# Optimization experiments

Hardware: AMD Instinct MI355X
Metric: run time of the kernel (lower is better)

## Reference

```python
import jax, jax.numpy as jnp
import numpy as np

H = 4
N = 50000
D_IN = 128
D_MODEL = 256
NCLASS = 40
B_S = 1
BH = B_S * H
LN_EPS = 1e-5


def sparse_perm_1D(indices, values, feats, n, bh):
    """Batched sparse (bh,n,n) @ dense (bh,n,d): gather -> scale -> segment-sum scatter."""
    gathered = feats[indices[0], indices[2]]              # (nnz, d)
    contrib = values[:, None] * gathered                   # (nnz, d)
    seg = indices[0] * n + indices[1]                      # (nnz,)
    out = jax.ops.segment_sum(contrib, seg, num_segments=bh * n)
    return out.reshape(bh, n, -1)


def layer_norm(x, gamma, beta):
    mu = jnp.mean(x, axis=-1, keepdims=True)
    var = jnp.var(x, axis=-1, keepdims=True)
    return (x - mu) * jax.lax.rsqrt(var + LN_EPS) * gamma + beta


def setup_inputs() -> dict:
    key = jax.random.key(0)
    k1, k2, k3, k4, k5, k6, k7 = jax.random.split(key, 7)
    # per-(batch*head) permutation sigma: nonzero at (b, i, sigma_b(i))
    perm_keys = jax.random.split(k1, BH)
    sigma = jax.vmap(lambda k: jax.random.permutation(k, N))(perm_keys)  # (BH, N)
    b_idx = jnp.repeat(jnp.arange(BH), N)
    row_idx = jnp.tile(jnp.arange(N), BH)
    col_idx = sigma.reshape(-1)
    perm_indices = jnp.stack([b_idx, row_idx, col_idx], axis=0).astype(jnp.int32)  # (3, BH*N)
    perm_values = jax.random.uniform(k2, (BH * N,), dtype=jnp.float32)
    features = jax.random.normal(k3, (B_S, N, D_IN), dtype=jnp.float32)
    appd = jax.random.normal(k4, (B_S, N, D_IN), dtype=jnp.float32)
    # parameters
    w_scale_in = 1.0 / np.sqrt(2 * D_IN)
    W_in = jax.random.uniform(k5, (2 * D_IN, D_MODEL), dtype=jnp.float32, minval=-w_scale_in, maxval=w_scale_in)
    b_in = jnp.zeros((D_MODEL,), dtype=jnp.float32)
    ln_gamma = jnp.ones((D_MODEL * H,), dtype=jnp.float32)
    ln_beta = jnp.zeros((D_MODEL * H,), dtype=jnp.float32)
    w_scale_h = 1.0 / np.sqrt(D_MODEL * H)
    W_head = jax.random.uniform(k6, (D_MODEL * H, NCLASS), dtype=jnp.float32, minval=-w_scale_h, maxval=w_scale_h)
    b_head = jax.random.uniform(k7, (NCLASS,), dtype=jnp.float32, minval=-w_scale_h, maxval=w_scale_h)
    return {"perm_indices": perm_indices, "perm_values": perm_values,
            "features": features, "appd": appd,
            "W_in": W_in, "b_in": b_in,
            "ln_gamma": ln_gamma, "ln_beta": ln_beta,
            "W_head": W_head, "b_head": b_head}


def reference(perm_indices, perm_values, features, appd, W_in, b_in, ln_gamma, ln_beta, W_head, b_head):
    # concat auxiliary features, replicate per head: (B_S,N,2*D_IN) -> (BH,N,2*D_IN)
    feat = jnp.concatenate([features, appd], axis=-1)
    feat = jnp.broadcast_to(feat[:, None], (B_S, H, N, 2 * D_IN)).reshape(BH, N, 2 * D_IN)
    # permute rows: perm @ feat
    x = sparse_perm_1D(perm_indices, perm_values, feat, N, BH)
    # ff_in + relu (dropout is identity at eval)
    x = jax.nn.relu(x @ W_in + b_in)                       # (BH, N, D_MODEL)
    # nlayers == nblocks == 0: compress/uncompress loops are empty
    # inverse permutation: perm^T @ x (swap row/col indices)
    idx_t = jnp.stack([perm_indices[0], perm_indices[2], perm_indices[1]], axis=0)
    y = sparse_perm_1D(idx_t, perm_values, x, N, BH)       # (BH, N, D_MODEL)
    # (B_S,H,N,D) -> (B_S,N,H*D)
    y = y.reshape(B_S, H, N, D_MODEL).transpose(0, 2, 1, 3).reshape(B_S, N, H * D_MODEL)
    y = layer_norm(y, ln_gamma, ln_beta)
    return y @ W_head + b_head                             # (B_S, N, NCLASS)
```

## Files before the change

kernel.cpp:

```cpp
#include <hip/hip_runtime.h>
#include <hip/hip_bf16.h>

#define NROW 50000
#define DIN 128
#define DM 256
#define HH 4
#define NC 40
#define BHN 200000
#define NBLK 3125

typedef float f32x4 __attribute__((ext_vector_type(4)));
typedef short bf16x8 __attribute__((ext_vector_type(8)));

__device__ __forceinline__ unsigned short f2bf(float x) {
    unsigned int u = __float_as_uint(x);
    u += 0x7fffu + ((u >> 16) & 1u);
    return (unsigned short)(u >> 16);
}

__device__ __forceinline__ unsigned int pk2(float lo, float hi) {
    __hip_bfloat162 h = __float22bfloat162_rn(make_float2(lo, hi));
    return *(unsigned int*)&h;
}

__device__ __forceinline__ float bf2f(unsigned short s) {
    return __uint_as_float(((unsigned int)s) << 16);
}

__global__ __launch_bounds__(256) void k_prep(const int* __restrict__ pi,
                                              const float* __restrict__ pv,
                                              const float* __restrict__ Win,
                                              const float* __restrict__ Wh,
                                              const float* __restrict__ gamma,
                                              const float* __restrict__ beta,
                                              const float* __restrict__ bh,
                                              float* __restrict__ vcol,
                                              unsigned short* __restrict__ Wpk,
                                              unsigned short* __restrict__ Wgpk,
                                              float* __restrict__ bias2) {
    const int bid = blockIdx.x, tid = threadIdx.x;
    if (bid < 782) {
        int k = bid * 256 + tid;
        if (k < BHN) {
            int b = (k >= 150000) ? 3 : (k >= 100000) ? 2 : (k >= 50000) ? 1 : 0;
            int col = pi[2 * BHN + k];
            vcol[b * NROW + col] = pv[k];
        }
    } else if (bid < 798) {
        int base = (bid - 782) * 512;
        #pragma unroll
        for (int q = 0; q < 2; ++q) {
            int s = base + q * 256 + tid;
            int ln = s & 63;
            int t  = (s >> 6) & 15;
            int kc = s >> 10;
            int n  = t * 16 + (ln & 15);
            int kb = kc * 32 + ((ln >> 4) << 3);
            union { unsigned int ui[4]; uint4 v4; } u;
            #pragma unroll
            for (int jj = 0; jj < 4; ++jj)
                u.ui[jj] = pk2(Win[(kb + 2 * jj) * DM + n], Win[(kb + 2 * jj + 1) * DM + n]);
            *(uint4*)&Wpk[s * 8] = u.v4;
        }
    } else if (bid < 810) {
        int base = (bid - 798) * 512;
        #pragma unroll
        for (int q = 0; q < 2; ++q) {
            int s = base + q * 256 + tid;
            int ln = s & 63;
            int u6 = s >> 6;
            int t  = u6 % 3;
            int v6 = u6 / 3;
            int kc = v6 & 7;
            int h  = v6 >> 3;
            int c  = t * 16 + (ln & 15);
            int d0 = h * 256 + kc * 32 + ((ln >> 4) << 3);
            union { unsigned int ui[4]; uint4 v4; } u;
            if (c < NC) {
                #pragma unroll
                for (int jj = 0; jj < 4; ++jj)
                    u.ui[jj] = pk2(gamma[d0 + 2 * jj] * Wh[(d0 + 2 * jj) * NC + c],
                                   gamma[d0 + 2 * jj + 1] * Wh[(d0 + 2 * jj + 1) * NC + c]);
            } else {
                u.v4 = make_uint4(0u, 0u, 0u, 0u);
            }
            *(uint4*)&Wgpk[s * 8] = u.v4;
        }
    } else {
        __shared__ float red[256];
        int c = bid - 810;
        float sb = 0.f;
        #pragma unroll
        for (int q = 0; q < 4; ++q) {
            int d = tid + 256 * q;
            sb = fmaf(beta[d], Wh[d * NC + c], sb);
        }
        red[tid] = sb;
        __syncthreads();
        for (int st = 128; st > 0; st >>= 1) {
            if (tid < st) red[tid] += red[tid + st];
            __syncthreads();
        }
        if (tid == 0) bias2[c] = bh[c] + red[0];
    }
}

__global__ __launch_bounds__(64, 3) void k_fused(
    const float* __restrict__ feats, const float* __restrict__ appd,
    const unsigned short* __restrict__ Wpk,
    const unsigned short* __restrict__ Wgpk,
    const float* __restrict__ vcol,
    const float* __restrict__ b_in,
    const float* __restrict__ bias2,
    float* __restrict__ out)
{
    __shared__ __align__(16) unsigned short Gb[16 * 264];
    __shared__ float rsS[16], nmS[16];

    const int tid = threadIdx.x;
    const int quad = tid >> 4;
    const int lr = tid & 15;
    const int j0 = blockIdx.x * 16;
    const int ar = j0 + lr;

    const f32x4 zero4 = {0.f, 0.f, 0.f, 0.f};

    f32x4 accG[16];
    #pragma unroll
    for (int t = 0; t < 16; ++t) accG[t] = zero4;

    #pragma unroll 1
    for (int kc = 0; kc < 8; ++kc) {
        const float* src = (kc < 4) ? feats : appd;
        const int ko = (kc & 3) * 32 + quad * 8;
        float4 x0 = *(const float4*)&src[(size_t)ar * DIN + ko];
        float4 x1 = *(const float4*)&src[(size_t)ar * DIN + ko + 4];
        union { unsigned int ui[4]; bf16x8 v; } a;
        a.ui[0] = pk2(x0.x, x0.y); a.ui[1] = pk2(x0.z, x0.w);
        a.ui[2] = pk2(x1.x, x1.y); a.ui[3] = pk2(x1.z, x1.w);
        #pragma unroll
        for (int t = 0; t < 16; ++t) {
            bf16x8 bf = *(const bf16x8*)&Wpk[(size_t)(((kc * 16 + t) << 6) + tid) * 8];
            accG[t] = __builtin_amdgcn_mfma_f32_16x16x32_bf16(a.v, bf, accG[t], 0, 0, 0);
        }
    }

    float vhh[HH][4];
    #pragma unroll
    for (int h = 0; h < HH; ++h)
        #pragma unroll
        for (int rg = 0; rg < 4; ++rg)
            vhh[h][rg] = vcol[h * NROW + j0 + quad * 4 + rg];

    float s_[4] = {0.f, 0.f, 0.f, 0.f}, ss_[4] = {0.f, 0.f, 0.f, 0.f};
    #pragma unroll
    for (int t = 0; t < 16; ++t) {
        float bt = b_in[t * 16 + lr];
        #pragma unroll
        for (int rg = 0; rg < 4; ++rg) {
            float gg = accG[t][rg];
            Gb[(quad * 4 + rg) * 264 + t * 16 + lr] = f2bf(gg);
            #pragma unroll
            for (int h = 0; h < HH; ++h) {
                float v = vhh[h][rg];
                float y = v * fmaxf(fmaf(v, gg, bt), 0.f);
                s_[rg] += y;
                ss_[rg] = fmaf(y, y, ss_[rg]);
            }
        }
    }
    #pragma unroll
    for (int m = 1; m <= 8; m <<= 1)
        #pragma unroll
        for (int rg = 0; rg < 4; ++rg) {
            s_[rg] += __shfl_xor(s_[rg], m);
            ss_[rg] += __shfl_xor(ss_[rg], m);
        }
    if (lr == 0) {
        #pragma unroll
        for (int rg = 0; rg < 4; ++rg) {
            float mm = s_[rg] * (1.f / 1024.f);
            float var = ss_[rg] * (1.f / 1024.f) - mm * mm;
            float r_ = rsqrtf(var + 1e-5f);
            rsS[quad * 4 + rg] = r_;
            nmS[quad * 4 + rg] = -mm * r_;
        }
    }
    __syncthreads();

    float vm[HH];
    #pragma unroll
    for (int h = 0; h < HH; ++h) vm[h] = vcol[h * NROW + ar];
    const float rsm = rsS[lr], nmm = nmS[lr];

    f32x4 accO[3];
    #pragma unroll
    for (int t = 0; t < 3; ++t) accO[t] = zero4;

    #pragma unroll 1
    for (int kc = 0; kc < 8; ++kc) {
        bf16x8 gf = *(const bf16x8*)&Gb[lr * 264 + kc * 32 + quad * 8];
        float4 bA = *(const float4*)&b_in[kc * 32 + quad * 8];
        float4 bB = *(const float4*)&b_in[kc * 32 + quad * 8 + 4];
        float bb[8] = {bA.x, bA.y, bA.z, bA.w, bB.x, bB.y, bB.z, bB.w};
        float g[8];
        #pragma unroll
        for (int j = 0; j < 8; ++j) g[j] = bf2f((unsigned short)gf[j]);
        #pragma unroll
        for (int h = 0; h < HH; ++h) {
            union { unsigned int ui[4]; bf16x8 v; } u;
            #pragma unroll
            for (int jj = 0; jj < 4; ++jj) {
                float ya = vm[h] * fmaxf(fmaf(vm[h], g[2 * jj], bb[2 * jj]), 0.f);
                float yb = vm[h] * fmaxf(fmaf(vm[h], g[2 * jj + 1], bb[2 * jj + 1]), 0.f);
                u.ui[jj] = pk2(fmaf(ya, rsm, nmm), fmaf(yb, rsm, nmm));
            }
            #pragma unroll
            for (int t = 0; t < 3; ++t) {
                bf16x8 wf = *(const bf16x8*)&Wgpk[(size_t)((((h * 8 + kc) * 3 + t) << 6) + tid) * 8];
                accO[t] = __builtin_amdgcn_mfma_f32_16x16x32_bf16(u.v, wf, accO[t], 0, 0, 0);
            }
        }
    }

    #pragma unroll
    for (int t = 0; t < 3; ++t) {
        int c = t * 16 + lr;
        if (c < NC) {
            float b2 = bias2[c];
            #pragma unroll
            for (int rg = 0; rg < 4; ++rg) {
                int row = j0 + quad * 4 + rg;
                out[(size_t)row * NC + c] = accO[t][rg] + b2;
            }
        }
    }
}

extern "C" void kernel_launch(void* const* d_in, const int* in_sizes, int n_in,
                              void* d_out, int out_size, void* d_ws, size_t ws_size,
                              hipStream_t stream) {
    const int*   pi    = (const int*)d_in[0];
    const float* pv    = (const float*)d_in[1];
    const float* feats = (const float*)d_in[2];
    const float* appd  = (const float*)d_in[3];
    const float* Win   = (const float*)d_in[4];
    const float* b_in  = (const float*)d_in[5];
    const float* gamma = (const float*)d_in[6];
    const float* beta  = (const float*)d_in[7];
    const float* Wh    = (const float*)d_in[8];
    const float* bh    = (const float*)d_in[9];
    float* out = (float*)d_out;

    char* w = (char*)d_ws;
    float*          vcolW  = (float*)w;
    unsigned short* WpkW   = (unsigned short*)(w + 800000);
    unsigned short* WgpkW  = (unsigned short*)(w + 931072);
    float*          bias2W = (float*)(w + 1029376);

    k_prep<<<850, 256, 0, stream>>>(pi, pv, Win, Wh, gamma, beta, bh, vcolW, WpkW, WgpkW, bias2W);
    k_fused<<<NBLK, 64, 0, stream>>>(feats, appd, WpkW, WgpkW, vcolW, b_in, bias2W, out);
}
```

Measured before the change: 148.1 us.

## Share staged weight tiles across four waves via direct global-to-LDS loads

Blocks grow from one wave handling 16 rows to four waves handling 64 rows. The packed W_in and head weights are staged once per block into LDS with global_load_lds and shared by all four waves, so each wave no longer streams the weights from global memory itself. The next feature chunk is prefetched while the current one is multiplied. In exchange the kernel adds block-wide barriers per chunk, uses more LDS (which can lower occupancy), and needs row clamping and guarded stores for the partial last block.

```diff
diff --git a/kernel.cpp b/kernel.cpp
--- a/kernel.cpp
+++ b/kernel.cpp
@@ -7,7 +7,7 @@
 #define HH 4
 #define NC 40
 #define BHN 200000
-#define NBLK 3125
+#define NBLK 782
 
 typedef float f32x4 __attribute__((ext_vector_type(4)));
 typedef short bf16x8 __attribute__((ext_vector_type(8)));
@@ -25,6 +25,13 @@
 
 __device__ __forceinline__ float bf2f(unsigned short s) {
     return __uint_as_float(((unsigned int)s) << 16);
+}
+
+__device__ __forceinline__ void gl_lds16(const unsigned short* g, unsigned short* l) {
+    __builtin_amdgcn_global_load_lds(
+        (const __attribute__((address_space(1))) unsigned int*)(g),
+        (__attribute__((address_space(3))) unsigned int*)(l),
+        16, 0, 0);
 }
 
 __global__ __launch_bounds__(256) void k_prep(const int* __restrict__ pi,
@@ -105,7 +112,7 @@
     }
 }
 
-__global__ __launch_bounds__(64, 3) void k_fused(
+__global__ __launch_bounds__(256, 3) void k_fused(
     const float* __restrict__ feats, const float* __restrict__ appd,
     const unsigned short* __restrict__ Wpk,
     const unsigned short* __restrict__ Wgpk,
@@ -114,33 +121,50 @@
     const float* __restrict__ bias2,
     float* __restrict__ out)
 {
-    __shared__ __align__(16) unsigned short Gb[16 * 264];
-    __shared__ float rsS[16], nmS[16];
+    __shared__ __align__(16) unsigned short stage[8192];
+    __shared__ __align__(16) unsigned short Gb[4][16 * 264];
+    __shared__ float rsS[4][16], nmS[4][16];
 
     const int tid = threadIdx.x;
-    const int quad = tid >> 4;
-    const int lr = tid & 15;
-    const int j0 = blockIdx.x * 16;
-    const int ar = j0 + lr;
+    const int wv = tid >> 6;
+    const int ln = tid & 63;
+    const int quad = ln >> 4;
+    const int lr = ln & 15;
+    const int j0 = blockIdx.x * 64;
+    const int jw = j0 + wv * 16;
+    const int ar = min(jw + lr, NROW - 1);
 
     const f32x4 zero4 = {0.f, 0.f, 0.f, 0.f};
 
     f32x4 accG[16];
     #pragma unroll
     for (int t = 0; t < 16; ++t) accG[t] = zero4;
+
+    float4 x0 = *(const float4*)&feats[(size_t)ar * DIN + quad * 8];
+    float4 x1 = *(const float4*)&feats[(size_t)ar * DIN + quad * 8 + 4];
 
     #pragma unroll 1
     for (int kc = 0; kc < 8; ++kc) {
-        const float* src = (kc < 4) ? feats : appd;
-        const int ko = (kc & 3) * 32 + quad * 8;
-        float4 x0 = *(const float4*)&src[(size_t)ar * DIN + ko];
-        float4 x1 = *(const float4*)&src[(size_t)ar * DIN + ko + 4];
+        __syncthreads();
+        #pragma unroll
+        for (int q = 0; q < 4; ++q) {
+            int f = wv * 4 + q;
+            gl_lds16(Wpk + ((size_t)((kc * 16 + f) * 64 + ln)) * 8, &stage[f * 512]);
+        }
+        __syncthreads();
+
         union { unsigned int ui[4]; bf16x8 v; } a;
         a.ui[0] = pk2(x0.x, x0.y); a.ui[1] = pk2(x0.z, x0.w);
         a.ui[2] = pk2(x1.x, x1.y); a.ui[3] = pk2(x1.z, x1.w);
+        if (kc < 7) {
+            const float* srcn = (kc + 1 < 4) ? feats : appd;
+            const int kon = ((kc + 1) & 3) * 32 + quad * 8;
+            x0 = *(const float4*)&srcn[(size_t)ar * DIN + kon];
+            x1 = *(const float4*)&srcn[(size_t)ar * DIN + kon + 4];
+        }
         #pragma unroll
         for (int t = 0; t < 16; ++t) {
-            bf16x8 bf = *(const bf16x8*)&Wpk[(size_t)(((kc * 16 + t) << 6) + tid) * 8];
+            bf16x8 bf = *(const bf16x8*)&stage[(t * 64 + ln) * 8];
             accG[t] = __builtin_amdgcn_mfma_f32_16x16x32_bf16(a.v, bf, accG[t], 0, 0, 0);
         }
     }
@@ -150,7 +174,7 @@
     for (int h = 0; h < HH; ++h)
         #pragma unroll
         for (int rg = 0; rg < 4; ++rg)
-            vhh[h][rg] = vcol[h * NROW + j0 + quad * 4 + rg];
+            vhh[h][rg] = vcol[h * NROW + min(jw + quad * 4 + rg, NROW - 1)];
 
     float s_[4] = {0.f, 0.f, 0.f, 0.f}, ss_[4] = {0.f, 0.f, 0.f, 0.f};
     #pragma unroll
@@ -159,7 +183,7 @@
         #pragma unroll
         for (int rg = 0; rg < 4; ++rg) {
             float gg = accG[t][rg];
-            Gb[(quad * 4 + rg) * 264 + t * 16 + lr] = f2bf(gg);
+            Gb[wv][(quad * 4 + rg) * 264 + t * 16 + lr] = f2bf(gg);
             #pragma unroll
             for (int h = 0; h < HH; ++h) {
                 float v = vhh[h][rg];
@@ -182,8 +206,8 @@
             float mm = s_[rg] * (1.f / 1024.f);
             float var = ss_[rg] * (1.f / 1024.f) - mm * mm;
             float r_ = rsqrtf(var + 1e-5f);
-            rsS[quad * 4 + rg] = r_;
-            nmS[quad * 4 + rg] = -mm * r_;
+            rsS[wv][quad * 4 + rg] = r_;
+            nmS[wv][quad * 4 + rg] = -mm * r_;
         }
     }
     __syncthreads();
@@ -191,36 +215,44 @@
     float vm[HH];
     #pragma unroll
     for (int h = 0; h < HH; ++h) vm[h] = vcol[h * NROW + ar];
-    const float rsm = rsS[lr], nmm = nmS[lr];
+    const float rsm = rsS[wv][lr], nmm = nmS[wv][lr];
 
     f32x4 accO[3];
     #pragma unroll
     for (int t = 0; t < 3; ++t) accO[t] = zero4;
 
     #pragma unroll 1
-    for (int kc = 0; kc < 8; ++kc) {
-        bf16x8 gf = *(const bf16x8*)&Gb[lr * 264 + kc * 32 + quad * 8];
-        float4 bA = *(const float4*)&b_in[kc * 32 + quad * 8];
-        float4 bB = *(const float4*)&b_in[kc * 32 + quad * 8 + 4];
-        float bb[8] = {bA.x, bA.y, bA.z, bA.w, bB.x, bB.y, bB.z, bB.w};
-        float g[8];
-        #pragma unroll
-        for (int j = 0; j < 8; ++j) g[j] = bf2f((unsigned short)gf[j]);
-        #pragma unroll
-        for (int h = 0; h < HH; ++h) {
+    for (int ch = 0; ch < 8; ++ch) {
+        const int h = ch >> 1;
+        const int k0 = (ch & 1) * 4;
+        #pragma unroll
+        for (int q = 0; q < 3; ++q) {
+            int s = wv * 3 + q;
+            gl_lds16(Wgpk + ((size_t)((((h * 8 + k0 + wv) * 3 + q)) * 64 + ln)) * 8,
+                     &stage[s * 512]);
+        }
+        __syncthreads();
+        #pragma unroll
+        for (int kcr = 0; kcr < 4; ++kcr) {
+            const int kc = k0 + kcr;
+            bf16x8 gf = *(const bf16x8*)&Gb[wv][lr * 264 + kc * 32 + quad * 8];
+            float4 bA = *(const float4*)&b_in[kc * 32 + quad * 8];
+            float4 bB = *(const float4*)&b_in[kc * 32 + quad * 8 + 4];
+            float bb[8] = {bA.x, bA.y, bA.z, bA.w, bB.x, bB.y, bB.z, bB.w};
             union { unsigned int ui[4]; bf16x8 v; } u;
             #pragma unroll
             for (int jj = 0; jj < 4; ++jj) {
-                float ya = vm[h] * fmaxf(fmaf(vm[h], g[2 * jj], bb[2 * jj]), 0.f);
-                float yb = vm[h] * fmaxf(fmaf(vm[h], g[2 * jj + 1], bb[2 * jj + 1]), 0.f);
+                float ya = vm[h] * fmaxf(fmaf(vm[h], bf2f((unsigned short)gf[2 * jj]), bb[2 * jj]), 0.f);
+                float yb = vm[h] * fmaxf(fmaf(vm[h], bf2f((unsigned short)gf[2 * jj + 1]), bb[2 * jj + 1]), 0.f);
                 u.ui[jj] = pk2(fmaf(ya, rsm, nmm), fmaf(yb, rsm, nmm));
             }
             #pragma unroll
             for (int t = 0; t < 3; ++t) {
-                bf16x8 wf = *(const bf16x8*)&Wgpk[(size_t)((((h * 8 + kc) * 3 + t) << 6) + tid) * 8];
+                bf16x8 wf = *(const bf16x8*)&stage[((kcr * 3 + t) * 64 + ln) * 8];
                 accO[t] = __builtin_amdgcn_mfma_f32_16x16x32_bf16(u.v, wf, accO[t], 0, 0, 0);
             }
         }
+        __syncthreads();
     }
 
     #pragma unroll
@@ -230,8 +262,9 @@
             float b2 = bias2[c];
             #pragma unroll
             for (int rg = 0; rg < 4; ++rg) {
-                int row = j0 + quad * 4 + rg;
-                out[(size_t)row * NC + c] = accO[t][rg] + b2;
+                int row = jw + quad * 4 + rg;
+                if (row < NROW)
+                    out[(size_t)row * NC + c] = accO[t][rg] + b2;
             }
         }
     }
@@ -259,5 +292,5 @@
     float*          bias2W = (float*)(w + 1029376);
 
     k_prep<<<850, 256, 0, stream>>>(pi, pv, Win, Wh, gamma, beta, bh, vcolW, WpkW, WgpkW, bias2W);
-    k_fused<<<NBLK, 64, 0, stream>>>(feats, appd, WpkW, WgpkW, vcolW, b_in, bias2W, out);
-}
+    k_fused<<<NBLK, 256, 0, stream>>>(feats, appd, WpkW, WgpkW, vcolW, b_in, bias2W, out);
+}
```

Measured after the change: 143.7 us. -3.0%, faster.
